# Kernel tuning notes

Measured on AMD Instinct MI355X. Metric: run time of the kernel, lower is better.

Reference implementation:

```python
import jax, jax.numpy as jnp
import numpy as np

B, D, N, R = 2048, 6, 256, 16


def setup_inputs() -> dict:
    key = jax.random.key(0)
    k_x, k_L, k_q, k_k, k_v, k_o = jax.random.split(key, 6)
    return {
        "x": jax.random.normal(k_x, (B, D, N), dtype=jnp.float32),
        "L": jax.random.normal(k_L, (B, N, N), dtype=jnp.float32),
        "Aq": jax.random.normal(k_q, (R, D), dtype=jnp.float32),
        "Ak": jax.random.normal(k_k, (R, D), dtype=jnp.float32),
        "Av": jax.random.normal(k_v, (R, D), dtype=jnp.float32),
        "Ao": jax.random.normal(k_o, (1, R), dtype=jnp.float32),
    }


def reference(x, L, Aq, Ak, Av, Ao):
    # numNeighbors: count of entries >= 1 in row 0 of each sample's L, plus 1
    numN = jnp.sum((L[:, 0, :] >= 1).astype(jnp.float32), axis=1).reshape(-1, 1, 1) + 1.0  # [B,1,1]
    # Q/K/V projections with tanh: [r,d] x [B,d,N] -> [B,r,N]
    Q = jnp.tanh(jnp.einsum("rd,bdn->brn", Aq, x))
    K = jnp.tanh(jnp.einsum("rd,bdn->brn", Ak, x))
    V = jnp.tanh(jnp.einsum("rd,bdn->brn", Av, x))
    # attention over the small r x r score matrix, scaled by sqrt(neighbor count)
    scores = jnp.einsum("brn,bsn->brs", Q, K) / jnp.sqrt(numN)  # [B,r,r]
    attn = jax.nn.softmax(scores, axis=2)
    o = jnp.einsum("brs,bsn->brn", attn, V)  # [B,r,N]
    H = jax.nn.silu(jnp.einsum("or,brn->bon", Ao, o))[:, 0, :]  # [B,N]
    return (jnp.sum(H, axis=1) ** 2)[:, None]  # [B,1]
```

## Files before the change

### kernel.cpp

```cpp
#include <hip/hip_runtime.h>

namespace {

constexpr int Dd   = 6;
constexpr int Nn   = 256;
constexpr int Rr   = 16;
constexpr int QSTR = 264;

typedef __attribute__((ext_vector_type(8))) short bf16x8;
typedef __attribute__((ext_vector_type(4))) float f32x4;

__device__ __forceinline__ float fast_tanh(float xv) {
  float e = __builtin_amdgcn_exp2f(xv * 2.8853900817779268f);
  return fmaf(-2.0f, __builtin_amdgcn_rcpf(e + 1.0f), 1.0f);
}

__device__ __forceinline__ unsigned pack_bf16(float a, float b) {
  unsigned r;
  asm("v_cvt_pk_bf16_f32 %0, %1, %2" : "=v"(r) : "v"(a), "v"(b));
  return r;
}

__global__ __launch_bounds__(256) void att_h_fused(
    const float* __restrict__ x,
    const float* __restrict__ L,
    const float* __restrict__ Aq,
    const float* __restrict__ Ak,
    const float* __restrict__ Av,
    const float* __restrict__ Ao,
    float* __restrict__ out)
{
  __shared__ __align__(16) unsigned short Qb[Rr * QSTR];
  __shared__ __align__(16) unsigned short Kb[Rr * QSTR];
  __shared__ __align__(16) float wsh[Rr];
  __shared__ float red[4];

  const int b    = blockIdx.x;
  const int tid  = threadIdx.x;
  const int wave = tid >> 6;
  const int lane = tid & 63;

  const float lv = L[(size_t)b * Nn * Nn + tid];
  const unsigned long long bal = __ballot(lv >= 1.0f);
  if (lane == 0) red[wave] = (float)__popcll(bal);

  const float* xb = x + (size_t)b * Dd * Nn;
  float xr[Dd];
#pragma unroll
  for (int d = 0; d < Dd; ++d) xr[d] = xb[d * Nn + tid];

  float q[Rr], k[Rr], v[Rr];
#pragma unroll
  for (int r = 0; r < Rr; ++r) {
    float aq = 0.0f, ak = 0.0f, av = 0.0f;
#pragma unroll
    for (int d = 0; d < Dd; ++d) {
      aq = fmaf(Aq[r * Dd + d], xr[d], aq);
      ak = fmaf(Ak[r * Dd + d], xr[d], ak);
      av = fmaf(Av[r * Dd + d], xr[d], av);
    }
    q[r] = fast_tanh(aq);
    k[r] = fast_tanh(ak);
    v[r] = fast_tanh(av);
  }

#pragma unroll
  for (int j = 0; j < 8; ++j) {
    const unsigned pq = pack_bf16(q[2 * j], q[2 * j + 1]);
    const unsigned pk = pack_bf16(k[2 * j], k[2 * j + 1]);
    Qb[(2 * j) * QSTR + tid]     = (unsigned short)pq;
    Qb[(2 * j + 1) * QSTR + tid] = (unsigned short)(pq >> 16);
    Kb[(2 * j) * QSTR + tid]     = (unsigned short)pk;
    Kb[(2 * j + 1) * QSTR + tid] = (unsigned short)(pk >> 16);
  }
  __syncthreads();

  if (wave == 0) {
    const float scale = rsqrtf(red[0] + red[1] + red[2] + red[3] + 1.0f);
    const int col = lane & 15;
    const int hi  = lane >> 4;
    const int off = hi * 8;

    f32x4 acc = {0.0f, 0.0f, 0.0f, 0.0f};
#pragma unroll
    for (int blk = 0; blk < 8; ++blk) {
      const bf16x8 af = *(const bf16x8*)&Qb[col * QSTR + blk * 32 + off];
      const bf16x8 bf = *(const bf16x8*)&Kb[col * QSTR + blk * 32 + off];
      acc = __builtin_amdgcn_mfma_f32_16x16x32_bf16(af, bf, acc, 0, 0, 0);
    }
    float att[4];
#pragma unroll
    for (int j = 0; j < 4; ++j) {
      const float sc = acc[j] * scale;
      float mj = sc;
#pragma unroll
      for (int o = 1; o < 16; o <<= 1) mj = fmaxf(mj, __shfl_xor(mj, o));
      const float ej = __builtin_amdgcn_exp2f((sc - mj) * 1.4426950408889634f);
      float sj = ej;
#pragma unroll
      for (int o = 1; o < 16; o <<= 1) sj += __shfl_xor(sj, o);
      att[j] = ej * __builtin_amdgcn_rcpf(sj);
    }
    const float4 ao4 = *(const float4*)(Ao + hi * 4);
    float wp = 0.0f;
    wp = fmaf(ao4.x, att[0], wp);
    wp = fmaf(ao4.y, att[1], wp);
    wp = fmaf(ao4.z, att[2], wp);
    wp = fmaf(ao4.w, att[3], wp);
    wp += __shfl_xor(wp, 16);
    wp += __shfl_xor(wp, 32);
    if (lane < Rr) wsh[lane] = wp;
  }
  __syncthreads();

  float h = 0.0f;
#pragma unroll
  for (int cg = 0; cg < 4; ++cg) {
    const float4 wv = *(const float4*)&wsh[4 * cg];
    h = fmaf(wv.x, v[4 * cg + 0], h);
    h = fmaf(wv.y, v[4 * cg + 1], h);
    h = fmaf(wv.z, v[4 * cg + 2], h);
    h = fmaf(wv.w, v[4 * cg + 3], h);
  }
  const float e  = __builtin_amdgcn_exp2f(-1.4426950408889634f * h);
  const float Hv = h * __builtin_amdgcn_rcpf(1.0f + e);

  float t = Hv;
#pragma unroll
  for (int o = 1; o < 64; o <<= 1) t += __shfl_xor(t, o);
  if (lane == 0) red[wave] = t;
  __syncthreads();
  if (tid == 0) {
    const float tot = red[0] + red[1] + red[2] + red[3];
    out[b] = tot * tot;
  }
}

}

extern "C" void kernel_launch(void* const* d_in, const int* in_sizes, int n_in,
                              void* d_out, int out_size, void* d_ws, size_t ws_size,
                              hipStream_t stream) {
  const float* x  = (const float*)d_in[0];
  const float* L  = (const float*)d_in[1];
  const float* Aq = (const float*)d_in[2];
  const float* Ak = (const float*)d_in[3];
  const float* Av = (const float*)d_in[4];
  const float* Ao = (const float*)d_in[5];
  float* out = (float*)d_out;

  const int B = in_sizes[0] / (Dd * Nn);
  att_h_fused<<<dim3(B), dim3(256), 0, stream>>>(x, L, Aq, Ak, Av, Ao, out);
}
```

Baseline: 17.02 us.

## Map one wave per sample and build MFMA operands in registers

Switches from one 256-thread block per sample to one 64-lane wave per sample, with four samples per block. This removes shared memory and all __syncthreads. Each lane computes Q/K tanh projections directly in the MFMA operand layout, so bf16 fragments are fed to MFMA without an LDS round trip, using two accumulators to break the dependency chain. V is recomputed per lane in the final stage, and reductions use only wave shuffles. Each wave now does 4x the per-thread work, and x is loaded twice, which adds redundant global traffic and ALU in exchange for no synchronization.

```diff
diff --git a/kernel.cpp b/kernel.cpp
--- a/kernel.cpp
+++ b/kernel.cpp
@@ -2,13 +2,13 @@
 
 namespace {
 
-constexpr int Dd   = 6;
-constexpr int Nn   = 256;
-constexpr int Rr   = 16;
-constexpr int QSTR = 264;
+constexpr int Dd = 6;
+constexpr int Nn = 256;
+constexpr int Rr = 16;
 
 typedef __attribute__((ext_vector_type(8))) short bf16x8;
 typedef __attribute__((ext_vector_type(4))) float f32x4;
+typedef __attribute__((ext_vector_type(4))) int i32x4;
 
 __device__ __forceinline__ float fast_tanh(float xv) {
   float e = __builtin_amdgcn_exp2f(xv * 2.8853900817779268f);
@@ -28,112 +28,118 @@
     const float* __restrict__ Ak,
     const float* __restrict__ Av,
     const float* __restrict__ Ao,
-    float* __restrict__ out)
+    float* __restrict__ out,
+    int B)
 {
-  __shared__ __align__(16) unsigned short Qb[Rr * QSTR];
-  __shared__ __align__(16) unsigned short Kb[Rr * QSTR];
-  __shared__ __align__(16) float wsh[Rr];
-  __shared__ float red[4];
+  const int tid  = threadIdx.x;
+  const int wv   = tid >> 6;
+  const int lane = tid & 63;
+  const int b    = blockIdx.x * 4 + wv;
+  if (b >= B) return;
 
-  const int b    = blockIdx.x;
-  const int tid  = threadIdx.x;
-  const int wave = tid >> 6;
-  const int lane = tid & 63;
+  const float* xb = x + (size_t)b * (Dd * Nn);
 
-  const float lv = L[(size_t)b * Nn * Nn + tid];
-  const unsigned long long bal = __ballot(lv >= 1.0f);
-  if (lane == 0) red[wave] = (float)__popcll(bal);
+  float xc[Dd][4];
+#pragma unroll
+  for (int d = 0; d < Dd; ++d) {
+    const float4 t = *(const float4*)(xb + d * Nn + lane * 4);
+    xc[d][0] = t.x; xc[d][1] = t.y; xc[d][2] = t.z; xc[d][3] = t.w;
+  }
 
-  const float* xb = x + (size_t)b * Dd * Nn;
-  float xr[Dd];
+  const float4 lr = *(const float4*)(L + (size_t)b * Nn * Nn + lane * 4);
+  float cnt = (float)(lr.x >= 1.0f) + (float)(lr.y >= 1.0f) +
+              (float)(lr.z >= 1.0f) + (float)(lr.w >= 1.0f);
 #pragma unroll
-  for (int d = 0; d < Dd; ++d) xr[d] = xb[d * Nn + tid];
+  for (int o = 1; o < 64; o <<= 1) cnt += __shfl_xor(cnt, o);
+  const float scale = rsqrtf(cnt + 1.0f);
 
-  float q[Rr], k[Rr], v[Rr];
+  const int r     = lane & 15;
+  const int quart = lane >> 4;
+  float aqr[Dd], akr[Dd];
 #pragma unroll
-  for (int r = 0; r < Rr; ++r) {
-    float aq = 0.0f, ak = 0.0f, av = 0.0f;
+  for (int p = 0; p < 3; ++p) {
+    const float2 a = *(const float2*)(Aq + r * Dd + 2 * p);
+    const float2 c = *(const float2*)(Ak + r * Dd + 2 * p);
+    aqr[2 * p] = a.x; aqr[2 * p + 1] = a.y;
+    akr[2 * p] = c.x; akr[2 * p + 1] = c.y;
+  }
+
+  f32x4 acc0 = {0.f, 0.f, 0.f, 0.f}, acc1 = {0.f, 0.f, 0.f, 0.f};
+#pragma unroll 2
+  for (int kb = 0; kb < 8; ++kb) {
+    const float* xw = xb + kb * 32 + quart * 8;
+    float xa[Dd][8];
 #pragma unroll
     for (int d = 0; d < Dd; ++d) {
-      aq = fmaf(Aq[r * Dd + d], xr[d], aq);
-      ak = fmaf(Ak[r * Dd + d], xr[d], ak);
-      av = fmaf(Av[r * Dd + d], xr[d], av);
+      const float4 t0 = *(const float4*)(xw + d * Nn);
+      const float4 t1 = *(const float4*)(xw + d * Nn + 4);
+      xa[d][0] = t0.x; xa[d][1] = t0.y; xa[d][2] = t0.z; xa[d][3] = t0.w;
+      xa[d][4] = t1.x; xa[d][5] = t1.y; xa[d][6] = t1.z; xa[d][7] = t1.w;
     }
-    q[r] = fast_tanh(aq);
-    k[r] = fast_tanh(ak);
-    v[r] = fast_tanh(av);
+    float qv[8], kv[8];
+#pragma unroll
+    for (int j = 0; j < 8; ++j) {
+      float aq = 0.0f, ak = 0.0f;
+#pragma unroll
+      for (int d = 0; d < Dd; ++d) {
+        aq = fmaf(aqr[d], xa[d][j], aq);
+        ak = fmaf(akr[d], xa[d][j], ak);
+      }
+      qv[j] = fast_tanh(aq);
+      kv[j] = fast_tanh(ak);
+    }
+    i32x4 qp, kp;
+#pragma unroll
+    for (int p = 0; p < 4; ++p) {
+      qp[p] = (int)pack_bf16(qv[2 * p], qv[2 * p + 1]);
+      kp[p] = (int)pack_bf16(kv[2 * p], kv[2 * p + 1]);
+    }
+    const bf16x8 qa = __builtin_bit_cast(bf16x8, qp);
+    const bf16x8 ka = __builtin_bit_cast(bf16x8, kp);
+    if (kb & 1)
+      acc1 = __builtin_amdgcn_mfma_f32_16x16x32_bf16(qa, ka, acc1, 0, 0, 0);
+    else
+      acc0 = __builtin_amdgcn_mfma_f32_16x16x32_bf16(qa, ka, acc0, 0, 0, 0);
   }
 
+  const float4 ao4 = *(const float4*)(Ao + quart * 4);
+  const float aoarr[4] = {ao4.x, ao4.y, ao4.z, ao4.w};
+  float wp = 0.0f;
 #pragma unroll
-  for (int j = 0; j < 8; ++j) {
-    const unsigned pq = pack_bf16(q[2 * j], q[2 * j + 1]);
-    const unsigned pk = pack_bf16(k[2 * j], k[2 * j + 1]);
-    Qb[(2 * j) * QSTR + tid]     = (unsigned short)pq;
-    Qb[(2 * j + 1) * QSTR + tid] = (unsigned short)(pq >> 16);
-    Kb[(2 * j) * QSTR + tid]     = (unsigned short)pk;
-    Kb[(2 * j + 1) * QSTR + tid] = (unsigned short)(pk >> 16);
+  for (int j = 0; j < 4; ++j) {
+    const float sc = (acc0[j] + acc1[j]) * scale;
+    float mj = sc;
+#pragma unroll
+    for (int o = 1; o < 16; o <<= 1) mj = fmaxf(mj, __shfl_xor(mj, o));
+    const float ej = __builtin_amdgcn_exp2f((sc - mj) * 1.4426950408889634f);
+    float sj = ej;
+#pragma unroll
+    for (int o = 1; o < 16; o <<= 1) sj += __shfl_xor(sj, o);
+    wp = fmaf(aoarr[j], ej * __builtin_amdgcn_rcpf(sj), wp);
   }
-  __syncthreads();
+  wp += __shfl_xor(wp, 16);
+  wp += __shfl_xor(wp, 32);
+  float wb[Rr];
+#pragma unroll
+  for (int s = 0; s < Rr; ++s) wb[s] = __shfl(wp, s);
 
-  if (wave == 0) {
-    const float scale = rsqrtf(red[0] + red[1] + red[2] + red[3] + 1.0f);
-    const int col = lane & 15;
-    const int hi  = lane >> 4;
-    const int off = hi * 8;
-
-    f32x4 acc = {0.0f, 0.0f, 0.0f, 0.0f};
+  float hsum = 0.0f;
 #pragma unroll
-    for (int blk = 0; blk < 8; ++blk) {
-      const bf16x8 af = *(const bf16x8*)&Qb[col * QSTR + blk * 32 + off];
-      const bf16x8 bf = *(const bf16x8*)&Kb[col * QSTR + blk * 32 + off];
-      acc = __builtin_amdgcn_mfma_f32_16x16x32_bf16(af, bf, acc, 0, 0, 0);
+  for (int c = 0; c < 4; ++c) {
+    float h = 0.0f;
+#pragma unroll
+    for (int s = 0; s < Rr; ++s) {
+      float av = 0.0f;
+#pragma unroll
+      for (int d = 0; d < Dd; ++d) av = fmaf(Av[s * Dd + d], xc[d][c], av);
+      h = fmaf(wb[s], fast_tanh(av), h);
     }
-    float att[4];
+    hsum += h * __builtin_amdgcn_rcpf(
+                    1.0f + __builtin_amdgcn_exp2f(-1.4426950408889634f * h));
+  }
 #pragma unroll
-    for (int j = 0; j < 4; ++j) {
-      const float sc = acc[j] * scale;
-      float mj = sc;
-#pragma unroll
-      for (int o = 1; o < 16; o <<= 1) mj = fmaxf(mj, __shfl_xor(mj, o));
-      const float ej = __builtin_amdgcn_exp2f((sc - mj) * 1.4426950408889634f);
-      float sj = ej;
-#pragma unroll
-      for (int o = 1; o < 16; o <<= 1) sj += __shfl_xor(sj, o);
-      att[j] = ej * __builtin_amdgcn_rcpf(sj);
-    }
-    const float4 ao4 = *(const float4*)(Ao + hi * 4);
-    float wp = 0.0f;
-    wp = fmaf(ao4.x, att[0], wp);
-    wp = fmaf(ao4.y, att[1], wp);
-    wp = fmaf(ao4.z, att[2], wp);
-    wp = fmaf(ao4.w, att[3], wp);
-    wp += __shfl_xor(wp, 16);
-    wp += __shfl_xor(wp, 32);
-    if (lane < Rr) wsh[lane] = wp;
-  }
-  __syncthreads();
-
-  float h = 0.0f;
-#pragma unroll
-  for (int cg = 0; cg < 4; ++cg) {
-    const float4 wv = *(const float4*)&wsh[4 * cg];
-    h = fmaf(wv.x, v[4 * cg + 0], h);
-    h = fmaf(wv.y, v[4 * cg + 1], h);
-    h = fmaf(wv.z, v[4 * cg + 2], h);
-    h = fmaf(wv.w, v[4 * cg + 3], h);
-  }
-  const float e  = __builtin_amdgcn_exp2f(-1.4426950408889634f * h);
-  const float Hv = h * __builtin_amdgcn_rcpf(1.0f + e);
-
-  float t = Hv;
-#pragma unroll
-  for (int o = 1; o < 64; o <<= 1) t += __shfl_xor(t, o);
-  if (lane == 0) red[wave] = t;
-  __syncthreads();
-  if (tid == 0) {
-    const float tot = red[0] + red[1] + red[2] + red[3];
-    out[b] = tot * tot;
-  }
+  for (int o = 1; o < 64; o <<= 1) hsum += __shfl_xor(hsum, o);
+  if (lane == 0) out[b] = hsum * hsum;
 }
 
 }
@@ -150,5 +156,5 @@
   float* out = (float*)d_out;
 
   const int B = in_sizes[0] / (Dd * Nn);
-  att_h_fused<<<dim3(B), dim3(256), 0, stream>>>(x, L, Aq, Ak, Av, Ao, out);
+  att_h_fused<<<dim3((B + 3) / 4), dim3(256), 0, stream>>>(x, L, Aq, Ak, Av, Ao, out, B);
 }
```

Measured after the change: 18.33 us. 1.08x slower.
